# Optimization experiments

Hardware: AMD Instinct MI355X
Metric: run time of the kernel (lower is better)

Reference implementation:

```python
import jax, jax.numpy as jnp
import numpy as np

K = 16  # knn_k
LN_EPS = 1e-5


def _layernorm(x, g, b):
    mu = jnp.mean(x, axis=-1, keepdims=True)
    var = jnp.var(x, axis=-1, keepdims=True)
    return (x - mu) * jax.lax.rsqrt(var + LN_EPS) * g + b


def _mlp_block(x, W1, b1, g, be, W2, b2):
    # Linear -> LayerNorm -> GELU -> Linear (MLPBlock)
    h = x @ W1 + b1
    h = jax.nn.gelu(_layernorm(h, g, be))
    return h @ W2 + b2


def _knn(v):
    # v: [N,3] -> indices of K nearest neighbors [N,K] (self included, as in knn search)
    sq = jnp.sum(v * v, axis=-1)                       # [N]
    d = sq[:, None] + sq[None, :] - 2.0 * (v @ v.T)    # [N,N] squared dists
    return jax.lax.top_k(-d, K)[1]                     # [N,K]


def setup_inputs() -> dict:
    key = jax.random.key(0)
    ks = jax.random.split(key, 8)
    B, N, C_IN, C_OUT, HID = 2, 8192, 32, 64, 128
    E_IN = C_IN + C_IN + 3  # 67
    s = 0.02
    return {
        "vertices": jax.random.normal(ks[0], (B, N, 3), jnp.float32),
        "features": jax.random.normal(ks[1], (B, N, C_IN), jnp.float32),
        "W1": jax.random.normal(ks[2], (E_IN, HID), jnp.float32) * s,
        "b1": jnp.zeros((HID,), jnp.float32),
        "g1": jnp.ones((HID,), jnp.float32),
        "be1": jnp.zeros((HID,), jnp.float32),
        "W2": jax.random.normal(ks[3], (HID, C_OUT), jnp.float32) * s,
        "b2": jnp.zeros((C_OUT,), jnp.float32),
        "Wo1": jax.random.normal(ks[4], (C_OUT, HID), jnp.float32) * s,
        "bo1": jnp.zeros((HID,), jnp.float32),
        "go": jnp.ones((HID,), jnp.float32),
        "beo": jnp.zeros((HID,), jnp.float32),
        "Wo2": jax.random.normal(ks[5], (HID, C_OUT), jnp.float32) * s,
        "bo2": jnp.zeros((C_OUT,), jnp.float32),
    }


def reference(vertices, features, W1, b1, g1, be1, W2, b2,
              Wo1, bo1, go, beo, Wo2, bo2):
    # out_point_feature_type == 'same': output points == input points
    idx = jax.vmap(_knn)(vertices)                                   # [B,N,K]
    gather = jax.vmap(lambda a, i: jnp.take(a, i, axis=0))
    neigh_feat = gather(features, idx)                               # [B,N,K,C]
    neigh_vert = gather(vertices, idx)                               # [B,N,K,3]
    self_feat = jnp.broadcast_to(features[:, :, None, :], neigh_feat.shape)
    rel_pos = neigh_vert - vertices[:, :, None, :]                   # [B,N,K,3]
    edge = jnp.concatenate([neigh_feat, self_feat, rel_pos], axis=-1)  # [B,N,K,2C+3]
    edge = _mlp_block(edge, W1, b1, g1, be1, W2, b2)                 # [B,N,K,C_out]
    out = jnp.mean(edge, axis=2)                                     # 'mean' reduction over K neighbors
    out = _mlp_block(out, Wo1, bo1, go, beo, Wo2, bo2)               # [B,N,C_out]
    return out
```

## Files before the change

kernel.cpp:

```cpp
#include <hip/hip_runtime.h>
#include <hip/hip_bf16.h>
#include <math.h>

#define BATCH 2
#define NPTS  8192
#define CIN   32
#define HID   128
#define COUT  64
#define EIN   67
#define KNN   16

#define TILE  1024
#define CAP   128
#define KMARGIN 1e-3f
#define KM_MFMA 4e-3f

typedef unsigned short u16;
typedef unsigned long long u64;
typedef __attribute__((ext_vector_type(8))) short bf16x8;
typedef __attribute__((ext_vector_type(4))) float f32x4;

#if defined(__has_builtin)
#if __has_builtin(__builtin_amdgcn_rcpf)
#define USE_RCPF 1
#endif
#endif

__device__ __forceinline__ u16 f2b(float f) {
    unsigned u = __float_as_uint(f);
    return (u16)((u + 0x7FFFu + ((u >> 16) & 1u)) >> 16);
}
__device__ __forceinline__ float b2f(u16 h) {
    return __uint_as_float(((unsigned)h) << 16);
}
__device__ __forceinline__ unsigned pk2(float a, float b) {
    return (unsigned)f2b(a) | ((unsigned)f2b(b) << 16);
}
__device__ __forceinline__ float gelu_t(float x) {
    float u = 1.5957691216057308f * (x + 0.044715f * x * x * x);
    float ex = __expf(u);
#ifdef USE_RCPF
    return x * ex * __builtin_amdgcn_rcpf(ex + 1.0f);
#else
    return x * ex / (ex + 1.0f);
#endif
}

__device__ __forceinline__ float rank16_of_64(float v, int lane) {
#pragma unroll
    for (int k = 2; k <= 64; k <<= 1) {
#pragma unroll
        for (int j = k >> 1; j > 0; j >>= 1) {
            float o = __shfl_xor(v, j, 64);
            bool lower = (lane & j) == 0;
            bool asc   = (lane & k) == 0;
            float mn = fminf(v, o), mx = fmaxf(v, o);
            v = (lower == asc) ? mn : mx;
        }
    }
    return __shfl(v, 15, 64);
}

__global__ void prep_kernel(const float* __restrict__ verts, float4* __restrict__ pv) {
    int i = blockIdx.x * blockDim.x + threadIdx.x;
    if (i >= BATCH * NPTS) return;
    float x = verts[3 * i], y = verts[3 * i + 1], z = verts[3 * i + 2];
    float sq = __fadd_rn(__fadd_rn(__fmul_rn(x, x), __fmul_rn(y, y)), __fmul_rn(z, z));
    pv[i] = make_float4(x, y, z, sq);
}

__global__ void prep2_kernel(const float* __restrict__ verts,
                             float4* __restrict__ pv, uint4* __restrict__ bfrag) {
    int i = blockIdx.x * blockDim.x + threadIdx.x;
    if (i >= BATCH * NPTS) return;
    float x = verts[3 * i], y = verts[3 * i + 1], z = verts[3 * i + 2];
    float sq = __fadd_rn(__fadd_rn(__fmul_rn(x, x), __fmul_rn(y, y)), __fmul_rn(z, z));
    pv[i] = make_float4(x, y, z, sq);

    u16 xh = f2b(x);  u16 xl = f2b(x - b2f(xh));
    u16 yh = f2b(y);  u16 yl = f2b(y - b2f(yh));
    u16 zh = f2b(z);  u16 zl = f2b(z - b2f(zh));
    u16 ch = f2b(sq); u16 cl = f2b(sq - b2f(ch));

    uint4 lo, hi;
    lo.x = (unsigned)xh | ((unsigned)xl << 16);
    lo.y = (unsigned)xh | ((unsigned)yh << 16);
    lo.z = (unsigned)yl | ((unsigned)yh << 16);
    lo.w = (unsigned)zh | ((unsigned)zl << 16);
    hi.x = (unsigned)zh | ((unsigned)ch << 16);
    hi.y = (unsigned)cl;
    hi.z = 0u; hi.w = 0u;
    bfrag[(size_t)i * 2]     = lo;
    bfrag[(size_t)i * 2 + 1] = hi;
}

__global__ __launch_bounds__(512, 8) void knn12_kernel(const float4* __restrict__ pv,
                                                       const uint4* __restrict__ bfrag,
                                                       int* __restrict__ nbr_out_rows) {
    __shared__ float mnsh[8][16][17];
    __shared__ float taus[16];
    __shared__ int   cnt[16];
    __shared__ int   sJ[16][CAP];
    __shared__ float bufD[16][CAP];

    const int tid = threadIdx.x, lane = tid & 63, wv = tid >> 6;
    const int col = lane & 15, qq = lane >> 4;
    const int ptb = blockIdx.x * 16;
    const int b = ptb >> 13, i0 = ptb & (NPTS - 1);
    const float4* __restrict__ P = pv + (size_t)b * NPTS;
    const uint4* __restrict__ BF = bfrag + (size_t)b * NPTS * 2;

    union U { uint4 u; bf16x8 v; };

    union { bf16x8 v; unsigned w[4]; } A;
    {
        float4 s = P[i0 + col];
        float mx = -2.0f * s.x, my = -2.0f * s.y, mz = -2.0f * s.z;
        u16 mxh = f2b(mx); u16 mxl = f2b(mx - b2f(mxh));
        u16 myh = f2b(my); u16 myl = f2b(my - b2f(myh));
        u16 mzh = f2b(mz); u16 mzl = f2b(mz - b2f(mzh));
        if (qq == 0) {
            A.w[0] = (unsigned)mxh | ((unsigned)mxh << 16);
            A.w[1] = (unsigned)mxl | ((unsigned)myh << 16);
            A.w[2] = (unsigned)myh | ((unsigned)myl << 16);
            A.w[3] = (unsigned)mzh | ((unsigned)mzh << 16);
        } else if (qq == 1) {
            A.w[0] = (unsigned)mzl | (0x3F80u << 16);
            A.w[1] = 0x3F80u;
            A.w[2] = 0u; A.w[3] = 0u;
        } else {
            A.w[0] = A.w[1] = A.w[2] = A.w[3] = 0u;
        }
    }

    const int cb = wv * 1024;
    const uint4* __restrict__ bp = BF + ((size_t)(cb + col) * 2 + (qq & 1));

    float mn0 = INFINITY, mn1 = INFINITY, mn2 = INFINITY, mn3 = INFINITY;
    for (int t = 0; t < 32; t += 2) {
        U b0, b1;
        b0.u = bp[(size_t)t * 32];
        b1.u = bp[(size_t)(t + 1) * 32];
        f32x4 a0 = (f32x4){0.f, 0.f, 0.f, 0.f};
        f32x4 a1 = (f32x4){0.f, 0.f, 0.f, 0.f};
        a0 = __builtin_amdgcn_mfma_f32_16x16x32_bf16(A.v, b0.v, a0, 0, 0, 0);
        a1 = __builtin_amdgcn_mfma_f32_16x16x32_bf16(A.v, b1.v, a1, 0, 0, 0);
        mn0 = fminf(mn0, fminf(a0[0], a1[0]));
        mn1 = fminf(mn1, fminf(a0[1], a1[1]));
        mn2 = fminf(mn2, fminf(a0[2], a1[2]));
        mn3 = fminf(mn3, fminf(a0[3], a1[3]));
    }
    mnsh[wv][qq * 4 + 0][col] = mn0;
    mnsh[wv][qq * 4 + 1][col] = mn1;
    mnsh[wv][qq * 4 + 2][col] = mn2;
    mnsh[wv][qq * 4 + 3][col] = mn3;
    if (tid < 16) cnt[tid] = 0;
    __syncthreads();

    {
        float tq[2];
#pragma unroll
        for (int q = 0; q < 2; ++q) {
            const int p = wv * 2 + q;
            float v = fminf(mnsh[lane >> 4][p][lane & 15],
                            mnsh[(lane >> 4) + 4][p][lane & 15]);
            tq[q] = rank16_of_64(v, lane) + KM_MFMA;
        }
        if (lane == 0) { taus[wv * 2] = tq[0]; taus[wv * 2 + 1] = tq[1]; }
    }
    __syncthreads();

    float mytau[4];
#pragma unroll
    for (int r = 0; r < 4; ++r) mytau[r] = taus[qq * 4 + r];

    for (int t = 0; t < 64; t += 2) {
        U b0, b1;
        b0.u = bp[(size_t)t * 32];
        b1.u = bp[(size_t)(t + 1) * 32];
        f32x4 a0 = (f32x4){0.f, 0.f, 0.f, 0.f};
        f32x4 a1 = (f32x4){0.f, 0.f, 0.f, 0.f};
        a0 = __builtin_amdgcn_mfma_f32_16x16x32_bf16(A.v, b0.v, a0, 0, 0, 0);
        a1 = __builtin_amdgcn_mfma_f32_16x16x32_bf16(A.v, b1.v, a1, 0, 0, 0);
        const int c0 = cb + t * 16 + col, c1 = c0 + 16;
        if ((a0[0] <= mytau[0]) | (a0[1] <= mytau[1]) |
            (a0[2] <= mytau[2]) | (a0[3] <= mytau[3]) |
            (a1[0] <= mytau[0]) | (a1[1] <= mytau[1]) |
            (a1[2] <= mytau[2]) | (a1[3] <= mytau[3])) {
#pragma unroll
            for (int r = 0; r < 4; ++r) {
                if (a0[r] <= mytau[r]) {
                    int p = qq * 4 + r;
                    int pos = atomicAdd(&cnt[p], 1);
                    if (pos < CAP) sJ[p][pos] = c0;
                }
                if (a1[r] <= mytau[r]) {
                    int p = qq * 4 + r;
                    int pos = atomicAdd(&cnt[p], 1);
                    if (pos < CAP) sJ[p][pos] = c1;
                }
            }
        }
    }
    __syncthreads();

#pragma unroll
    for (int q = 0; q < 2; ++q) {
        const int p = wv * 2 + q;
        int ns = cnt[p]; ns = (ns > CAP) ? CAP : ns;
        const float4 sp = P[i0 + p];
        float dl[2]; int jl[2];
#pragma unroll
        for (int slot = 0; slot < 2; ++slot) {
            int sidx = slot * 64 + lane;
            bool act = sidx < ns;
            int js = act ? sJ[p][sidx] : 0;
            float4 cc = P[js];
            float dot = __fmul_rn(sp.x, cc.x);
            dot = __fmaf_rn(sp.y, cc.y, dot);
            dot = __fmaf_rn(sp.z, cc.z, dot);
            float d = __fsub_rn(__fadd_rn(sp.w, cc.w), __fmul_rn(2.0f, dot));
            if (act) bufD[p][sidx] = d;
            dl[slot] = d; jl[slot] = js;
        }
        int r0 = 0, r1 = 0;
        for (int mm = 0; mm < ns; ++mm) {
            float dm = bufD[p][mm]; int jm = sJ[p][mm];
            r0 += (dm < dl[0]) || (dm == dl[0] && jm < jl[0]);
            r1 += (dm < dl[1]) || (dm == dl[1] && jm < jl[1]);
        }
        if (lane < ns && r0 < KNN)
            nbr_out_rows[(size_t)(ptb + p) * 64 + r0] = jl[0];
        if (64 + lane < ns && r1 < KNN)
            nbr_out_rows[(size_t)(ptb + p) * 64 + r1] = jl[1];
    }
}

__global__ __launch_bounds__(256, 8) void knn9_kernel(const float4* __restrict__ pv,
                                                      int* __restrict__ nbr_out_rows) {
    __shared__ float  bufD[4][2][CAP];
    __shared__ int    bufJ[4][2][CAP];

    const int tid = threadIdx.x, lane = tid & 63, wv = tid >> 6;
    const int pt0 = (blockIdx.x * 4 + wv) * 2;
    const int b = pt0 >> 13, i0 = pt0 & (NPTS - 1);
    const float4* P = pv + (size_t)b * NPTS;

    float4 sp[2];
    float ax[2], ay[2], az[2];
#pragma unroll
    for (int p = 0; p < 2; ++p) {
        sp[p] = P[i0 + p];
        ax[p] = -2.0f * sp[p].x; ay[p] = -2.0f * sp[p].y; az[p] = -2.0f * sp[p].z;
    }

    float mn[2] = {INFINITY, INFINITY};
    for (int t = 0; t < 16; ++t) {
        float4 c0 = P[t * 256 + lane];
        float4 c1 = P[t * 256 + 64 + lane];
        float4 c2 = P[t * 256 + 128 + lane];
        float4 c3 = P[t * 256 + 192 + lane];
#pragma unroll
        for (int p = 0; p < 2; ++p) {
            float f0 = __fmaf_rn(ax[p], c0.x, __fmaf_rn(ay[p], c0.y, __fmaf_rn(az[p], c0.z, c0.w)));
            float f1 = __fmaf_rn(ax[p], c1.x, __fmaf_rn(ay[p], c1.y, __fmaf_rn(az[p], c1.z, c1.w)));
            float f2 = __fmaf_rn(ax[p], c2.x, __fmaf_rn(ay[p], c2.y, __fmaf_rn(az[p], c2.z, c2.w)));
            float f3 = __fmaf_rn(ax[p], c3.x, __fmaf_rn(ay[p], c3.y, __fmaf_rn(az[p], c3.z, c3.w)));
            mn[p] = fminf(fminf(fminf(mn[p], f0), fminf(f1, f2)), f3);
        }
    }

    float tau[2];
#pragma unroll
    for (int p = 0; p < 2; ++p)
        tau[p] = rank16_of_64(mn[p], lane) + KMARGIN;

    int base[2] = {0, 0};
    for (int t = 0; t < 32; ++t) {
        float4 c[4];
#pragma unroll
        for (int k = 0; k < 4; ++k) c[k] = P[t * 256 + k * 64 + lane];
        bool pr[4][2];
        bool anyl = false;
#pragma unroll
        for (int k = 0; k < 4; ++k)
#pragma unroll
            for (int p = 0; p < 2; ++p) {
                float f = __fmaf_rn(ax[p], c[k].x,
                          __fmaf_rn(ay[p], c[k].y,
                          __fmaf_rn(az[p], c[k].z, c[k].w)));
                pr[k][p] = (f <= tau[p]);
                anyl |= pr[k][p];
            }
        if (__ballot(anyl) == 0ull) continue;
#pragma unroll
        for (int k = 0; k < 4; ++k) {
            u64 anyk = __ballot(pr[k][0] | pr[k][1]);
            if (anyk == 0ull) continue;
            int j = t * 256 + k * 64 + lane;
#pragma unroll
            for (int p = 0; p < 2; ++p) {
                u64 mk = __ballot(pr[k][p]);
                if (mk != 0ull) {
                    if (pr[k][p]) {
                        int pos = base[p] + (int)__popcll(mk & ((1ull << lane) - 1ull));
                        if (pos < CAP) bufJ[wv][p][pos] = j;
                    }
                    base[p] += (int)__popcll(mk);
                }
            }
        }
    }

#pragma unroll
    for (int p = 0; p < 2; ++p) {
        int ns = base[p]; ns = (ns > CAP) ? CAP : ns;
        float dloc[2]; int jloc[2];
#pragma unroll
        for (int slot = 0; slot < 2; ++slot) {
            int sidx = slot * 64 + lane;
            bool act = sidx < ns;
            int js = act ? bufJ[wv][p][sidx] : 0;
            float4 cc = P[js];
            float dot = __fmul_rn(sp[p].x, cc.x);
            dot = __fmaf_rn(sp[p].y, cc.y, dot);
            dot = __fmaf_rn(sp[p].z, cc.z, dot);
            float d = __fsub_rn(__fadd_rn(sp[p].w, cc.w), __fmul_rn(2.0f, dot));
            if (act) bufD[wv][p][sidx] = d;
            dloc[slot] = d; jloc[slot] = js;
        }
        int r0 = 0, r1 = 0;
        for (int mm = 0; mm < ns; ++mm) {
            float dm = bufD[wv][p][mm]; int jm = bufJ[wv][p][mm];
            r0 += (dm < dloc[0]) || (dm == dloc[0] && jm < jloc[0]);
            r1 += (dm < dloc[1]) || (dm == dloc[1] && jm < jloc[1]);
        }
        if (lane < ns && r0 < KNN)
            nbr_out_rows[(size_t)(pt0 + p) * 64 + r0] = jloc[0];
        if (64 + lane < ns && r1 < KNN)
            nbr_out_rows[(size_t)(pt0 + p) * 64 + r1] = jloc[1];
    }
}

__global__ __launch_bounds__(256) void knn_kernel(const float* __restrict__ verts,
                                                  int* nbr_out_rows) {
    __shared__ float4 tilebuf[TILE];
    __shared__ float  bufD[4][CAP];
    __shared__ int    bufJ[4][CAP];

    const int tid = threadIdx.x, lane = tid & 63, wv = tid >> 6;
    const int pt = blockIdx.x * 4 + wv;
    const int b = pt >> 13, i = pt & (NPTS - 1);
    const float* vb = verts + (size_t)b * NPTS * 3;

    const float xi = vb[3 * i], yi = vb[3 * i + 1], zi = vb[3 * i + 2];
    const float sqi = __fadd_rn(__fadd_rn(__fmul_rn(xi, xi), __fmul_rn(yi, yi)),
                                __fmul_rn(zi, zi));

    float m_d = INFINITY;
    for (int t = 0; t < NPTS / TILE; ++t) {
        __syncthreads();
        for (int s = 0; s < TILE / 256; ++s) {
            int p = t * TILE + s * 256 + tid;
            float px = vb[3 * p], py = vb[3 * p + 1], pz = vb[3 * p + 2];
            float sq = __fadd_rn(__fadd_rn(__fmul_rn(px, px), __fmul_rn(py, py)),
                                 __fmul_rn(pz, pz));
            tilebuf[s * 256 + tid] = make_float4(px, py, pz, sq);
        }
        __syncthreads();
        for (int it = 0; it < TILE / 64; ++it) {
            float4 c = tilebuf[it * 64 + lane];
            float dot = __fmul_rn(xi, c.x);
            dot = __fmaf_rn(yi, c.y, dot);
            dot = __fmaf_rn(zi, c.z, dot);
            float d = __fsub_rn(__fadd_rn(sqi, c.w), __fmul_rn(2.0f, dot));
            m_d = fminf(m_d, d);
        }
    }
    __shared__ float minv[4][64];
    minv[wv][lane] = m_d;
    __syncthreads();
    int rnk = 0;
    for (int mm = 0; mm < 64; ++mm) {
        float vm = minv[wv][mm];
        rnk += (vm < m_d) || (vm == m_d && mm < lane);
    }
    u64 bal = __ballot(rnk == 15);
    float tau = __shfl(m_d, __ffsll(bal) - 1, 64);

    int base = 0;
    for (int t = 0; t < NPTS / TILE; ++t) {
        __syncthreads();
        for (int s = 0; s < TILE / 256; ++s) {
            int p = t * TILE + s * 256 + tid;
            float px = vb[3 * p], py = vb[3 * p + 1], pz = vb[3 * p + 2];
            float sq = __fadd_rn(__fadd_rn(__fmul_rn(px, px), __fmul_rn(py, py)),
                                 __fmul_rn(pz, pz));
            tilebuf[s * 256 + tid] = make_float4(px, py, pz, sq);
        }
        __syncthreads();
        for (int it = 0; it < TILE / 64; ++it) {
            int jl = it * 64 + lane;
            float4 c = tilebuf[jl];
            float dot = __fmul_rn(xi, c.x);
            dot = __fmaf_rn(yi, c.y, dot);
            dot = __fmaf_rn(zi, c.z, dot);
            float d = __fsub_rn(__fadd_rn(sqi, c.w), __fmul_rn(2.0f, dot));
            bool pred = (d <= tau);
            u64 mask = __ballot(pred);
            if (pred) {
                int pos = base + (int)__popcll(mask & ((1ull << lane) - 1ull));
                if (pos < CAP) { bufD[wv][pos] = d; bufJ[wv][pos] = t * TILE + jl; }
            }
            base += (int)__popcll(mask);
        }
    }
    int ns = (base > CAP) ? CAP : base;
    __syncthreads();
#pragma unroll
    for (int slot = 0; slot < 2; ++slot) {
        int sidx = slot * 64 + lane;
        if (sidx < ns) {
            float ds = bufD[wv][sidx];
            int   js = bufJ[wv][sidx];
            int rank = 0;
            for (int mm = 0; mm < ns; ++mm) {
                float dm = bufD[wv][mm];
                int   jm = bufJ[wv][mm];
                rank += (dm < ds) || (dm == ds && jm < js);
            }
            if (rank < KNN) nbr_out_rows[(size_t)pt * 64 + rank] = js;
        }
    }
}

__global__ __launch_bounds__(512, 2) void edge8_kernel(
    const float* __restrict__ verts, const float* __restrict__ feats,
    const float* __restrict__ W1, const float* __restrict__ b1,
    const float* __restrict__ g1, const float* __restrict__ be1,
    const float* __restrict__ W2, const float* __restrict__ b2,
    const float* __restrict__ Wo1, const float* __restrict__ bo1,
    const float* __restrict__ go_, const float* __restrict__ beo,
    const float* __restrict__ Wo2, const float* __restrict__ bo2,
    float* out)
{
    __shared__ u16 EPw[8][4][64][8];
    __shared__ u16 W1F[3][8][64][8];
    __shared__ u16 W2F[4][4][64][8];
    __shared__ float b1s[HID], g1s[HID], be1s[HID];
    __shared__ float b2s[COUT];
    __shared__ float meansh[32][68];

    const int tid  = threadIdx.x;
    const int lane = tid & 63, wv = tid >> 6;
    const int quad = lane >> 4, n16 = lane & 15;

    for (int s = tid; s < 3 * 8 * 64; s += 512) {
        int kt = s >> 9, nt = (s >> 6) & 7, ln = s & 63;
        int q = ln >> 4, nn = ln & 15;
        int col = nt * 16 + nn;
        union { bf16x8 v; unsigned u[4]; } pk;
#pragma unroll
        for (int jj = 0; jj < 4; ++jj) {
            int k0 = kt * 32 + q * 8 + jj * 2;
            float a  = (k0     < EIN) ? W1[(size_t)k0 * HID + col]       : 0.0f;
            float bq = (k0 + 1 < EIN) ? W1[(size_t)(k0 + 1) * HID + col] : 0.0f;
            pk.u[jj] = pk2(a, bq);
        }
        *(bf16x8*)&W1F[kt][nt][ln][0] = pk.v;
    }
    for (int s = tid; s < 4 * 4 * 64; s += 512) {
        int kt2 = s >> 8, nt2 = (s >> 6) & 3, ln = s & 63;
        int q = ln >> 4, nn = ln & 15;
        int o = nt2 * 16 + nn;
        union { bf16x8 v; unsigned u[4]; } pk;
#pragma unroll
        for (int jj = 0; jj < 4; ++jj) {
            int k0 = kt2 * 32 + q * 8 + jj * 2;
            pk.u[jj] = pk2(W2[(size_t)k0 * COUT + o],
                           W2[(size_t)(k0 + 1) * COUT + o]);
        }
        *(bf16x8*)&W2F[kt2][nt2][ln][0] = pk.v;
    }
    if (tid < HID) { b1s[tid] = b1[tid]; g1s[tid] = g1[tid]; be1s[tid] = be1[tid]; }
    if (tid >= HID && tid < HID + COUT) b2s[tid - HID] = b2[tid - HID];
    __syncthreads();

    const int ptb = blockIdx.x * 32;
    const int bb  = ptb >> 13;
    const float* fb  = feats + (size_t)bb * NPTS * CIN;
    const float* vbk = verts + (size_t)bb * NPTS * 3;
    const int ptw = ptb + wv * 4;
    const int ipw = ptw & (NPTS - 1);

    float b1v[8], g1v[8], bev[8];
#pragma unroll
    for (int nt = 0; nt < 8; ++nt) {
        b1v[nt] = b1s[nt * 16 + n16];
        g1v[nt] = g1s[nt * 16 + n16];
        bev[nt] = be1s[nt * 16 + n16];
    }

    const int k16 = lane & 15;
    const int qq  = lane >> 4;

    int jnv[4];
#pragma unroll
    for (int pp = 0; pp < 4; ++pp)
        jnv[pp] = ((const int*)out)[(size_t)(ptw + pp) * 64 + k16];

    float4 nA, nB, sA, sB;
    float rx = 0.f, ry = 0.f, rz = 0.f;
    {
        const int jn = jnv[0], ipn = ipw;
        const float* nsrc = fb + (size_t)jn * CIN + qq * 8;
        nA = *(const float4*)nsrc; nB = *(const float4*)(nsrc + 4);
        const float* ssrc = fb + (size_t)ipn * CIN + qq * 8;
        sA = *(const float4*)ssrc; sB = *(const float4*)(ssrc + 4);
        if (qq == 0) {
            rx = vbk[3 * jn]     - vbk[3 * ipn];
            ry = vbk[3 * jn + 1] - vbk[3 * ipn + 1];
            rz = vbk[3 * jn + 2] - vbk[3 * ipn + 2];
        }
    }

#pragma unroll
    for (int pp = 0; pp < 4; ++pp) {
        {
            union { bf16x8 v; unsigned u[4]; } e0, e1, e2;
            e0.u[0] = pk2(nA.x, nA.y); e0.u[1] = pk2(nA.z, nA.w);
            e0.u[2] = pk2(nB.x, nB.y); e0.u[3] = pk2(nB.z, nB.w);
            e1.u[0] = pk2(sA.x, sA.y); e1.u[1] = pk2(sA.z, sA.w);
            e1.u[2] = pk2(sB.x, sB.y); e1.u[3] = pk2(sB.z, sB.w);
            e2.u[0] = e2.u[1] = e2.u[2] = e2.u[3] = 0u;
            if (qq == 0) { e2.u[0] = pk2(rx, ry); e2.u[1] = pk2(rz, 0.0f); }
            *(bf16x8*)&EPw[wv][0][lane][0] = e0.v;
            *(bf16x8*)&EPw[wv][1][lane][0] = e1.v;
            *(bf16x8*)&EPw[wv][2][lane][0] = e2.v;
        }

        if (pp < 3) {
            const int jn = jnv[pp + 1], ipn = ipw + pp + 1;
            const float* nsrc = fb + (size_t)jn * CIN + qq * 8;
            nA = *(const float4*)nsrc; nB = *(const float4*)(nsrc + 4);
            const float* ssrc = fb + (size_t)ipn * CIN + qq * 8;
            sA = *(const float4*)ssrc; sB = *(const float4*)(ssrc + 4);
            if (qq == 0) {
                rx = vbk[3 * jn]     - vbk[3 * ipn];
                ry = vbk[3 * jn + 1] - vbk[3 * ipn + 1];
                rz = vbk[3 * jn + 2] - vbk[3 * ipn + 2];
            }
        }

        f32x4 acc[8];
#pragma unroll
        for (int nt = 0; nt < 8; ++nt) acc[nt] = (f32x4){0.f, 0.f, 0.f, 0.f};
#pragma unroll
        for (int kt = 0; kt < 3; ++kt) {
            bf16x8 a = *(bf16x8*)&EPw[wv][kt][lane][0];
#pragma unroll
            for (int nt = 0; nt < 8; ++nt) {
                bf16x8 bfr = *(bf16x8*)&W1F[kt][nt][lane][0];
                acc[nt] = __builtin_amdgcn_mfma_f32_16x16x32_bf16(a, bfr, acc[nt], 0, 0, 0);
            }
        }

        float s1[4] = {0,0,0,0}, s2[4] = {0,0,0,0};
#pragma unroll
        for (int nt = 0; nt < 8; ++nt)
#pragma unroll
            for (int r = 0; r < 4; ++r) {
                float x = acc[nt][r] + b1v[nt];
                s1[r] += x; s2[r] += x * x;
            }
#pragma unroll
        for (int r = 0; r < 4; ++r) {
#pragma unroll
            for (int off = 1; off < 16; off <<= 1) {
                s1[r] += __shfl_xor(s1[r], off, 64);
                s2[r] += __shfl_xor(s2[r], off, 64);
            }
        }
        float mu[4], rs[4];
#pragma unroll
        for (int r = 0; r < 4; ++r) {
            mu[r] = s1[r] * (1.0f / HID);
            float var = s2[r] * (1.0f / HID) - mu[r] * mu[r];
            rs[r] = rsqrtf(var + 1e-5f);
        }

#pragma unroll
        for (int nt = 0; nt < 8; ++nt) {
            int kt2 = nt >> 1;
            int q2  = (nt * 2 + (n16 >> 3)) & 3;
            int jj  = n16 & 7;
#pragma unroll
            for (int r = 0; r < 4; ++r) {
                float x  = acc[nt][r] + b1v[nt];
                float xn = (x - mu[r]) * rs[r] * g1v[nt] + bev[nt];
                EPw[wv][kt2][quad * 4 + r + 16 * q2][jj] = (u16)f2b(gelu_t(xn));
            }
        }

        f32x4 acc2[4];
#pragma unroll
        for (int nt2 = 0; nt2 < 4; ++nt2) acc2[nt2] = (f32x4){0.f, 0.f, 0.f, 0.f};
#pragma unroll
        for (int kt2 = 0; kt2 < 4; ++kt2) {
            bf16x8 a2 = *(bf16x8*)&EPw[wv][kt2][lane][0];
#pragma unroll
            for (int nt2 = 0; nt2 < 4; ++nt2) {
                bf16x8 bfr2 = *(bf16x8*)&W2F[kt2][nt2][lane][0];
                acc2[nt2] = __builtin_amdgcn_mfma_f32_16x16x32_bf16(a2, bfr2, acc2[nt2], 0, 0, 0);
            }
        }

#pragma unroll
        for (int nt2 = 0; nt2 < 4; ++nt2) {
            float cs = acc2[nt2][0] + acc2[nt2][1] + acc2[nt2][2] + acc2[nt2][3];
            cs += __shfl_xor(cs, 16, 64);
            cs += __shfl_xor(cs, 32, 64);
            if (quad == 0) {
                int o = nt2 * 16 + n16;
                meansh[wv * 4 + pp][o] = cs * (1.0f / KNN) + b2s[o];
            }
        }
    }

    __syncthreads();

    for (int s = tid; s < 2 * 8 * 64; s += 512) {
        int kt = s >> 9, nt = (s >> 6) & 7, ln = s & 63;
        int q = ln >> 4, nn = ln & 15;
        int col = nt * 16 + nn;
        union { bf16x8 v; unsigned u[4]; } pk;
#pragma unroll
        for (int jj = 0; jj < 4; ++jj) {
            int k0 = kt * 32 + q * 8 + jj * 2;
            pk.u[jj] = pk2(Wo1[(size_t)k0 * HID + col],
                           Wo1[(size_t)(k0 + 1) * HID + col]);
        }
        *(bf16x8*)&W1F[kt][nt][ln][0] = pk.v;
    }
    for (int s = tid; s < 4 * 4 * 64; s += 512) {
        int kt2 = s >> 8, nt2 = (s >> 6) & 3, ln = s & 63;
        int q = ln >> 4, nn = ln & 15;
        int o = nt2 * 16 + nn;
        union { bf16x8 v; unsigned u[4]; } pk;
#pragma unroll
        for (int jj = 0; jj < 4; ++jj) {
            int k0 = kt2 * 32 + q * 8 + jj * 2;
            pk.u[jj] = pk2(Wo2[(size_t)k0 * COUT + o],
                           Wo2[(size_t)(k0 + 1) * COUT + o]);
        }
        *(bf16x8*)&W2F[kt2][nt2][ln][0] = pk.v;
    }
    if (tid < HID) { b1s[tid] = bo1[tid]; g1s[tid] = go_[tid]; be1s[tid] = beo[tid]; }
    if (tid >= HID && tid < HID + COUT) b2s[tid - HID] = bo2[tid - HID];
    __syncthreads();

    if (wv < 2) {
        const int pr0 = wv * 16;
        bf16x8 af[2];
#pragma unroll
        for (int kt = 0; kt < 2; ++kt) {
            const float* mrow = &meansh[pr0 + n16][kt * 32 + quad * 8];
            float4 A = *(const float4*)mrow, B4 = *(const float4*)(mrow + 4);
            union { bf16x8 v; unsigned u[4]; } pk;
            pk.u[0] = pk2(A.x, A.y); pk.u[1] = pk2(A.z, A.w);
            pk.u[2] = pk2(B4.x, B4.y); pk.u[3] = pk2(B4.z, B4.w);
            af[kt] = pk.v;
        }

        f32x4 acc[8];
#pragma unroll
        for (int nt = 0; nt < 8; ++nt) acc[nt] = (f32x4){0.f, 0.f, 0.f, 0.f};
#pragma unroll
        for (int kt = 0; kt < 2; ++kt)
#pragma unroll
            for (int nt = 0; nt < 8; ++nt) {
                bf16x8 bfr = *(bf16x8*)&W1F[kt][nt][lane][0];
                acc[nt] = __builtin_amdgcn_mfma_f32_16x16x32_bf16(af[kt], bfr, acc[nt], 0, 0, 0);
            }

        float pb1[8], pg1[8], pbe[8];
#pragma unroll
        for (int nt = 0; nt < 8; ++nt) {
            pb1[nt] = b1s[nt * 16 + n16];
            pg1[nt] = g1s[nt * 16 + n16];
            pbe[nt] = be1s[nt * 16 + n16];
        }
        float s1[4] = {0,0,0,0}, s2[4] = {0,0,0,0};
#pragma unroll
        for (int nt = 0; nt < 8; ++nt)
#pragma unroll
            for (int r = 0; r < 4; ++r) {
                float x = acc[nt][r] + pb1[nt];
                s1[r] += x; s2[r] += x * x;
            }
#pragma unroll
        for (int r = 0; r < 4; ++r) {
#pragma unroll
            for (int off = 1; off < 16; off <<= 1) {
                s1[r] += __shfl_xor(s1[r], off, 64);
                s2[r] += __shfl_xor(s2[r], off, 64);
            }
        }
#pragma unroll
        for (int nt = 0; nt < 8; ++nt) {
            int kt2 = nt >> 1;
            int q2  = (nt * 2 + (n16 >> 3)) & 3;
            int jj  = n16 & 7;
#pragma unroll
            for (int r = 0; r < 4; ++r) {
                float mu = s1[r] * (1.0f / HID);
                float var = s2[r] * (1.0f / HID) - mu * mu;
                float rs = rsqrtf(var + 1e-5f);
                float x  = acc[nt][r] + pb1[nt];
                float xn = (x - mu) * rs * pg1[nt] + pbe[nt];
                EPw[wv][kt2][quad * 4 + r + 16 * q2][jj] = (u16)f2b(gelu_t(xn));
            }
        }

        f32x4 acc2[4];
#pragma unroll
        for (int nt2 = 0; nt2 < 4; ++nt2) acc2[nt2] = (f32x4){0.f, 0.f, 0.f, 0.f};
#pragma unroll
        for (int kt2 = 0; kt2 < 4; ++kt2) {
            bf16x8 a2 = *(bf16x8*)&EPw[wv][kt2][lane][0];
#pragma unroll
            for (int nt2 = 0; nt2 < 4; ++nt2) {
                bf16x8 bfr2 = *(bf16x8*)&W2F[kt2][nt2][lane][0];
                acc2[nt2] = __builtin_amdgcn_mfma_f32_16x16x32_bf16(a2, bfr2, acc2[nt2], 0, 0, 0);
            }
        }

#pragma unroll
        for (int nt2 = 0; nt2 < 4; ++nt2) {
            int o = nt2 * 16 + n16;
#pragma unroll
            for (int r = 0; r < 4; ++r)
                meansh[pr0 + quad * 4 + r][o] = acc2[nt2][r] + b2s[o];
        }
    }
    __syncthreads();

    {
        int p = tid >> 4, c = (tid & 15) * 4;
        float4 v = *(const float4*)&meansh[p][c];
        *(float4*)&out[(size_t)(ptb + p) * 64 + c] = v;
    }
}

extern "C" void kernel_launch(void* const* d_in, const int* in_sizes, int n_in,
                              void* d_out, int out_size, void* d_ws, size_t ws_size,
                              hipStream_t stream) {
    const float* verts = (const float*)d_in[0];
    const float* feats = (const float*)d_in[1];
    const float* W1  = (const float*)d_in[2];
    const float* b1  = (const float*)d_in[3];
    const float* g1  = (const float*)d_in[4];
    const float* be1 = (const float*)d_in[5];
    const float* W2  = (const float*)d_in[6];
    const float* b2  = (const float*)d_in[7];
    const float* Wo1 = (const float*)d_in[8];
    const float* bo1 = (const float*)d_in[9];
    const float* go_ = (const float*)d_in[10];
    const float* beo = (const float*)d_in[11];
    const float* Wo2 = (const float*)d_in[12];
    const float* bo2 = (const float*)d_in[13];
    float* out = (float*)d_out;

    (void)in_sizes; (void)n_in; (void)out_size;

    const size_t pv_bytes = (size_t)BATCH * NPTS * sizeof(float4);
    const size_t bf_bytes = (size_t)BATCH * NPTS * 32;
    if (ws_size >= pv_bytes + bf_bytes) {
        float4* pv = (float4*)d_ws;
        uint4*  bf = (uint4*)((char*)d_ws + pv_bytes);
        prep2_kernel<<<(BATCH * NPTS + 255) / 256, 256, 0, stream>>>(verts, pv, bf);
        knn12_kernel<<<(BATCH * NPTS) / 16, 512, 0, stream>>>(pv, bf, (int*)out);
    } else if (ws_size >= pv_bytes) {
        float4* pv = (float4*)d_ws;
        prep_kernel<<<(BATCH * NPTS + 255) / 256, 256, 0, stream>>>(verts, pv);
        knn9_kernel<<<(BATCH * NPTS) / 8, 256, 0, stream>>>(pv, (int*)out);
    } else {
        knn_kernel<<<(BATCH * NPTS) / 4, 256, 0, stream>>>(verts, (int*)out);
    }
    edge8_kernel<<<(BATCH * NPTS) / 32, 512, 0, stream>>>(
        verts, feats, W1, b1, g1, be1, W2, b2,
        Wo1, bo1, go_, beo, Wo2, bo2, out);
}
```

Baseline: 185.8 us.

## Switch KNN distance MFMA to 32x32x16 tiles with 32 queries per block

The KNN candidate search moves from 16x16x32 bf16 MFMA (16 queries per block, half of the K lanes padded with zeros) to 32x32x16 MFMA processing 32 query points per block. Each candidate-fragment load is now reused across twice as many queries, and the K dimension is no longer half wasted. Per-thread atomics for candidate insertion are replaced by a wave ballot with one leader atomic per row segment plus a popcount prefix. In exchange it uses more registers and shared memory, launch bounds drop to 2 blocks per SM, and there are half as many blocks.

```diff
diff --git a/kernel.cpp b/kernel.cpp
--- a/kernel.cpp
+++ b/kernel.cpp
@@ -19,6 +19,7 @@
 typedef unsigned long long u64;
 typedef __attribute__((ext_vector_type(8))) short bf16x8;
 typedef __attribute__((ext_vector_type(4))) float f32x4;
+typedef __attribute__((ext_vector_type(16))) float f32x16;
 
 #if defined(__has_builtin)
 #if __has_builtin(__builtin_amdgcn_rcpf)
@@ -94,18 +95,18 @@
     bfrag[(size_t)i * 2 + 1] = hi;
 }
 
-__global__ __launch_bounds__(512, 8) void knn12_kernel(const float4* __restrict__ pv,
+__global__ __launch_bounds__(512, 2) void knn14_kernel(const float4* __restrict__ pv,
                                                        const uint4* __restrict__ bfrag,
                                                        int* __restrict__ nbr_out_rows) {
-    __shared__ float mnsh[8][16][17];
-    __shared__ float taus[16];
-    __shared__ int   cnt[16];
-    __shared__ int   sJ[16][CAP];
-    __shared__ float bufD[16][CAP];
+    __shared__ float mnsh[8][32][8];
+    __shared__ float taus[32];
+    __shared__ int   cnt[32];
+    __shared__ int   sJ[32][CAP];
+    __shared__ float bufD[32][CAP];
 
     const int tid = threadIdx.x, lane = tid & 63, wv = tid >> 6;
-    const int col = lane & 15, qq = lane >> 4;
-    const int ptb = blockIdx.x * 16;
+    const int cc32 = lane & 31, h = lane >> 5;
+    const int ptb = blockIdx.x * 32;
     const int b = ptb >> 13, i0 = ptb & (NPTS - 1);
     const float4* __restrict__ P = pv + (size_t)b * NPTS;
     const uint4* __restrict__ BF = bfrag + (size_t)b * NPTS * 2;
@@ -114,99 +115,95 @@
 
     union { bf16x8 v; unsigned w[4]; } A;
     {
-        float4 s = P[i0 + col];
+        float4 s = P[i0 + cc32];
         float mx = -2.0f * s.x, my = -2.0f * s.y, mz = -2.0f * s.z;
         u16 mxh = f2b(mx); u16 mxl = f2b(mx - b2f(mxh));
         u16 myh = f2b(my); u16 myl = f2b(my - b2f(myh));
         u16 mzh = f2b(mz); u16 mzl = f2b(mz - b2f(mzh));
-        if (qq == 0) {
+        if (h == 0) {
             A.w[0] = (unsigned)mxh | ((unsigned)mxh << 16);
             A.w[1] = (unsigned)mxl | ((unsigned)myh << 16);
             A.w[2] = (unsigned)myh | ((unsigned)myl << 16);
             A.w[3] = (unsigned)mzh | ((unsigned)mzh << 16);
-        } else if (qq == 1) {
+        } else {
             A.w[0] = (unsigned)mzl | (0x3F80u << 16);
             A.w[1] = 0x3F80u;
             A.w[2] = 0u; A.w[3] = 0u;
-        } else {
-            A.w[0] = A.w[1] = A.w[2] = A.w[3] = 0u;
         }
     }
 
     const int cb = wv * 1024;
-    const uint4* __restrict__ bp = BF + ((size_t)(cb + col) * 2 + (qq & 1));
-
-    float mn0 = INFINITY, mn1 = INFINITY, mn2 = INFINITY, mn3 = INFINITY;
-    for (int t = 0; t < 32; t += 2) {
-        U b0, b1;
-        b0.u = bp[(size_t)t * 32];
-        b1.u = bp[(size_t)(t + 1) * 32];
-        f32x4 a0 = (f32x4){0.f, 0.f, 0.f, 0.f};
-        f32x4 a1 = (f32x4){0.f, 0.f, 0.f, 0.f};
-        a0 = __builtin_amdgcn_mfma_f32_16x16x32_bf16(A.v, b0.v, a0, 0, 0, 0);
-        a1 = __builtin_amdgcn_mfma_f32_16x16x32_bf16(A.v, b1.v, a1, 0, 0, 0);
-        mn0 = fminf(mn0, fminf(a0[0], a1[0]));
-        mn1 = fminf(mn1, fminf(a0[1], a1[1]));
-        mn2 = fminf(mn2, fminf(a0[2], a1[2]));
-        mn3 = fminf(mn3, fminf(a0[3], a1[3]));
-    }
-    mnsh[wv][qq * 4 + 0][col] = mn0;
-    mnsh[wv][qq * 4 + 1][col] = mn1;
-    mnsh[wv][qq * 4 + 2][col] = mn2;
-    mnsh[wv][qq * 4 + 3][col] = mn3;
-    if (tid < 16) cnt[tid] = 0;
+    const uint4* __restrict__ bp = BF + ((size_t)(cb + cc32) * 2 + h);
+
+    float mn[16];
+#pragma unroll
+    for (int r = 0; r < 16; ++r) mn[r] = INFINITY;
+    for (int t = 0; t < 16; ++t) {
+        U bu; bu.u = bp[(size_t)t * 64];
+        f32x16 acc = (f32x16)(0.0f);
+        acc = __builtin_amdgcn_mfma_f32_32x32x16_bf16(A.v, bu.v, acc, 0, 0, 0);
+#pragma unroll
+        for (int r = 0; r < 16; ++r) mn[r] = fminf(mn[r], acc[r]);
+    }
+#pragma unroll
+    for (int r = 0; r < 16; ++r) {
+        float v = mn[r];
+        v = fminf(v, __shfl_xor(v, 8, 64));
+        v = fminf(v, __shfl_xor(v, 16, 64));
+        if ((lane & 24) == 0) {
+            int row = (r & 3) + 8 * (r >> 2) + 4 * h;
+            mnsh[wv][row][lane & 7] = v;
+        }
+    }
+    if (tid < 32) cnt[tid] = 0;
     __syncthreads();
 
     {
-        float tq[2];
-#pragma unroll
-        for (int q = 0; q < 2; ++q) {
-            const int p = wv * 2 + q;
-            float v = fminf(mnsh[lane >> 4][p][lane & 15],
-                            mnsh[(lane >> 4) + 4][p][lane & 15]);
-            tq[q] = rank16_of_64(v, lane) + KM_MFMA;
-        }
-        if (lane == 0) { taus[wv * 2] = tq[0]; taus[wv * 2 + 1] = tq[1]; }
-    }
-    __syncthreads();
-
-    float mytau[4];
-#pragma unroll
-    for (int r = 0; r < 4; ++r) mytau[r] = taus[qq * 4 + r];
-
-    for (int t = 0; t < 64; t += 2) {
-        U b0, b1;
-        b0.u = bp[(size_t)t * 32];
-        b1.u = bp[(size_t)(t + 1) * 32];
-        f32x4 a0 = (f32x4){0.f, 0.f, 0.f, 0.f};
-        f32x4 a1 = (f32x4){0.f, 0.f, 0.f, 0.f};
-        a0 = __builtin_amdgcn_mfma_f32_16x16x32_bf16(A.v, b0.v, a0, 0, 0, 0);
-        a1 = __builtin_amdgcn_mfma_f32_16x16x32_bf16(A.v, b1.v, a1, 0, 0, 0);
-        const int c0 = cb + t * 16 + col, c1 = c0 + 16;
-        if ((a0[0] <= mytau[0]) | (a0[1] <= mytau[1]) |
-            (a0[2] <= mytau[2]) | (a0[3] <= mytau[3]) |
-            (a1[0] <= mytau[0]) | (a1[1] <= mytau[1]) |
-            (a1[2] <= mytau[2]) | (a1[3] <= mytau[3])) {
-#pragma unroll
-            for (int r = 0; r < 4; ++r) {
-                if (a0[r] <= mytau[r]) {
-                    int p = qq * 4 + r;
-                    int pos = atomicAdd(&cnt[p], 1);
-                    if (pos < CAP) sJ[p][pos] = c0;
+#pragma unroll
+        for (int q = 0; q < 4; ++q) {
+            const int p = wv * 4 + q;
+            float v = mnsh[lane >> 3][p][lane & 7];
+            float tq = rank16_of_64(v, lane) + KM_MFMA;
+            if (lane == 0) taus[p] = tq;
+        }
+    }
+    __syncthreads();
+
+    float mytau[16];
+#pragma unroll
+    for (int r = 0; r < 16; ++r)
+        mytau[r] = taus[(r & 3) + 8 * (r >> 2) + 4 * h];
+
+    for (int t = 0; t < 32; ++t) {
+        U bu; bu.u = bp[(size_t)t * 64];
+        f32x16 acc = (f32x16)(0.0f);
+        acc = __builtin_amdgcn_mfma_f32_32x32x16_bf16(A.v, bu.v, acc, 0, 0, 0);
+        const int cbase = cb + t * 32;
+#pragma unroll
+        for (int r = 0; r < 16; ++r) {
+            bool pred = (acc[r] <= mytau[r]);
+            u64 mk = __ballot(pred);
+            if (mk != 0ull) {
+                unsigned seg = (unsigned)(mk >> (h * 32));
+                if (seg) {
+                    const int p = (r & 3) + 8 * (r >> 2) + 4 * h;
+                    int leader = (h << 5) + (__ffs(seg) - 1);
+                    int base = 0;
+                    if (lane == leader) base = atomicAdd(&cnt[p], (int)__popc(seg));
+                    base = __shfl(base, leader, 64);
+                    if (pred) {
+                        int pos = base + (int)__popc(seg & ((1u << cc32) - 1u));
+                        if (pos < CAP) sJ[p][pos] = cbase + cc32;
+                    }
                 }
-                if (a1[r] <= mytau[r]) {
-                    int p = qq * 4 + r;
-                    int pos = atomicAdd(&cnt[p], 1);
-                    if (pos < CAP) sJ[p][pos] = c1;
-                }
-            }
-        }
-    }
-    __syncthreads();
-
-#pragma unroll
-    for (int q = 0; q < 2; ++q) {
-        const int p = wv * 2 + q;
+            }
+        }
+    }
+    __syncthreads();
+
+#pragma unroll
+    for (int q = 0; q < 4; ++q) {
+        const int p = wv * 4 + q;
         int ns = cnt[p]; ns = (ns > CAP) ? CAP : ns;
         const float4 sp = P[i0 + p];
         float dl[2]; int jl[2];
@@ -779,7 +776,7 @@
         float4* pv = (float4*)d_ws;
         uint4*  bf = (uint4*)((char*)d_ws + pv_bytes);
         prep2_kernel<<<(BATCH * NPTS + 255) / 256, 256, 0, stream>>>(verts, pv, bf);
-        knn12_kernel<<<(BATCH * NPTS) / 16, 512, 0, stream>>>(pv, bf, (int*)out);
+        knn14_kernel<<<(BATCH * NPTS) / 32, 512, 0, stream>>>(pv, bf, (int*)out);
     } else if (ws_size >= pv_bytes) {
         float4* pv = (float4*)d_ws;
         prep_kernel<<<(BATCH * NPTS + 255) / 256, 256, 0, stream>>>(verts, pv);
```

After: 389.4 us. 2.1x slower.
